# Optimization experiments

Hardware: AMD Instinct MI355X
Metric: run time of the kernel (lower is better)

## Reference

```python
import jax, jax.numpy as jnp
import numpy as np

B = 64            # decode batch (one new token per sequence)
H = 32            # query heads
HKV = 2           # kv heads (multi_query_group_num)
D = 128           # head_size (kv_channels)
HID = 4096        # hidden size
ROT = D // 2      # ChatGLM applies rotary to first half of head dims
BLOCK = 16        # paged-cache block size
NBLK = 16384      # total blocks
MAX_S = 4096
ROPE_BASE = 10000.0


def setup_inputs() -> dict:
    key = jax.random.key(0)
    ks = jax.random.split(key, 8)
    hidden_states = jax.random.normal(ks[0], (B, HID), jnp.float32)
    wqkv = jax.random.normal(ks[1], (H * D + 2 * HKV * D, HID), jnp.float32) * 0.02
    wdense = jax.random.normal(ks[2], (HID, H * D), jnp.float32) * 0.02
    k_cache = jax.random.normal(ks[3], (NBLK, BLOCK, HKV, D), jnp.float32)
    v_cache = jax.random.normal(ks[4], (NBLK, BLOCK, HKV, D), jnp.float32)
    # disjoint block tables: sequence b owns blocks [b*256, (b+1)*256)
    block_tables = jnp.arange(B * (MAX_S // BLOCK), dtype=jnp.int32).reshape(B, MAX_S // BLOCK)
    input_lengths = jax.random.randint(ks[5], (B,), 1024, MAX_S + 1, dtype=jnp.int32)
    # slot of the current token = position input_lengths-1 within its block table
    pos = input_lengths - 1
    slots = block_tables[jnp.arange(B), pos // BLOCK] * BLOCK + pos % BLOCK
    return {"hidden_states": hidden_states, "wqkv": wqkv, "wdense": wdense,
            "k_cache": k_cache, "v_cache": v_cache, "block_tables": block_tables,
            "slots": slots, "input_lengths": input_lengths, "max_s": MAX_S}


def _apply_rope(x, positions):
    # x: [B, h, D]; GPT-J interleaved rope on first ROT dims (ChatGLM style)
    inv_freq = 1.0 / (ROPE_BASE ** (jnp.arange(0, ROT, 2, dtype=jnp.float32) / ROT))  # [ROT/2]
    ang = positions.astype(jnp.float32)[:, None] * inv_freq[None, :]                  # [B, ROT/2]
    c = jnp.cos(ang)[:, None, :]  # [B,1,ROT/2]
    s = jnp.sin(ang)[:, None, :]
    xr = x[..., :ROT].reshape(*x.shape[:-1], ROT // 2, 2)
    x0, x1 = xr[..., 0], xr[..., 1]
    rot = jnp.stack([x0 * c - x1 * s, x1 * c + x0 * s], axis=-1).reshape(*x.shape[:-1], ROT)
    return jnp.concatenate([rot, x[..., ROT:]], axis=-1)


def reference(hidden_states, wqkv, wdense, k_cache, v_cache, block_tables, slots, input_lengths, max_s):
    G = H // HKV
    scale = D ** -0.5
    positions = input_lengths - 1

    qkv = hidden_states @ wqkv.T                                   # [B, 4608]
    q, k, v = jnp.split(qkv, [H * D, H * D + HKV * D], axis=1)
    q = q.reshape(B, H, D)
    k = k.reshape(B, HKV, D)
    v = v.reshape(B, HKV, D)

    q = _apply_rope(q, positions)
    k = _apply_rope(k, positions)

    # reshape_and_cache: scatter current token's K/V into the paged cache
    kc = k_cache.reshape(NBLK * BLOCK, HKV, D).at[slots].set(k)
    vc = v_cache.reshape(NBLK * BLOCK, HKV, D).at[slots].set(v)

    # paged attention: gather per-sequence KV via block tables
    s_idx = jnp.arange(max_s)
    flat = block_tables[:, s_idx // BLOCK] * BLOCK + s_idx % BLOCK  # [B, S]
    K = kc[flat]                                                    # [B, S, HKV, D]
    V = vc[flat]

    q4 = q.reshape(B, HKV, G, D).astype(jnp.float32)
    scores = jnp.einsum('bkgd,bskd->bkgs', q4, K.astype(jnp.float32)) * scale  # [B,HKV,G,S]
    mask = s_idx[None, :] < input_lengths[:, None]                  # [B, S]
    scores = jnp.where(mask[:, None, None, :], scores, -jnp.inf)
    probs = jax.nn.softmax(scores, axis=-1)
    out = jnp.einsum('bkgs,bskd->bkgd', probs, V.astype(jnp.float32))  # [B,HKV,G,D]
    out = out.reshape(B, H * D).astype(hidden_states.dtype)
    return out @ wdense.T
```

## Files before the change

kernel.cpp:

```cpp
#include <hip/hip_runtime.h>
#include <math.h>

#define KDIM 4096
#define SPLITS 8
#define WAYS 32
#define MAXPB 256
#define NQKV 4608
#define NDENSE 4096
#define KSPLIT 8
#define KRANGE 512

typedef __attribute__((ext_vector_type(8))) short bh8;
typedef __attribute__((ext_vector_type(4))) float f32x4;

__device__ __forceinline__ short f2bf(float x) {
    union { float f; unsigned u; } v; v.f = x;
    unsigned r = v.u + 0x7FFFu + ((v.u >> 16) & 1u);
    return (short)(r >> 16);
}
__device__ __forceinline__ float bf2f(short h) {
    union { unsigned u; float f; } v;
    v.u = ((unsigned)(unsigned short)h) << 16;
    return v.f;
}

__device__ __forceinline__ void rope_rotate(float& x0, float& x1, int j, int pos) {
    double inv = pow(10000.0, -(double)j / 32.0);
    double ang = (double)pos * inv;
    float c = (float)cos(ang), s = (float)sin(ang);
    float r0 = x0 * c - x1 * s;
    float r1 = x1 * c + x0 * s;
    x0 = r0; x1 = r1;
}

__global__ __launch_bounds__(256) void prep_hilo(
    const float* __restrict__ x, unsigned short* __restrict__ hi,
    unsigned short* __restrict__ lo)
{
    const int i = (blockIdx.x * 256 + threadIdx.x) * 4;
    float4 v = *(const float4*)&x[i];
    unsigned short h4[4], l4[4];
    float vf[4] = {v.x, v.y, v.z, v.w};
    #pragma unroll
    for (int j = 0; j < 4; ++j) {
        short hh = f2bf(vf[j]);
        h4[j] = (unsigned short)hh;
        l4[j] = (unsigned short)f2bf(vf[j] - bf2f(hh));
    }
    *(ushort4*)&hi[i] = make_ushort4(h4[0], h4[1], h4[2], h4[3]);
    *(ushort4*)&lo[i] = make_ushort4(l4[0], l4[1], l4[2], l4[3]);
}

__global__ __launch_bounds__(256) void gemm_mfma(
    const unsigned short* __restrict__ A_hi, const unsigned short* __restrict__ A_lo,
    const float* __restrict__ W, float* __restrict__ part, int N)
{
    const int tid = threadIdx.x;
    const int wv = tid >> 6;
    const int l = tid & 63;
    const int lr = l & 15;
    const int h = l >> 4;
    const int n0 = blockIdx.x * 64 + wv * 16;
    const int k0 = blockIdx.y * KRANGE;

    const float* wrow = &W[(size_t)(n0 + lr) * KDIM + h * 8];
    const unsigned short* pah[4];
    const unsigned short* pal[4];
    #pragma unroll
    for (int mt = 0; mt < 4; ++mt) {
        pah[mt] = &A_hi[(mt * 16 + lr) * KDIM + h * 8];
        pal[mt] = &A_lo[(mt * 16 + lr) * KDIM + h * 8];
    }

    f32x4 acc[4];
    #pragma unroll
    for (int mt = 0; mt < 4; ++mt) acc[mt] = (f32x4){0.f, 0.f, 0.f, 0.f};

    float4 wc0, wc1, wn0, wn1;
    bh8 ahc[4], alc[4], ahn[4], aln[4];

    wc0 = *(const float4*)&wrow[k0];
    wc1 = *(const float4*)&wrow[k0 + 4];
    #pragma unroll
    for (int mt = 0; mt < 4; ++mt) {
        ahc[mt] = *(const bh8*)&pah[mt][k0];
        alc[mt] = *(const bh8*)&pal[mt][k0];
    }

    for (int kt = 0; kt < KRANGE / 32; ++kt) {
        if (kt + 1 < KRANGE / 32) {
            const int kn = k0 + (kt + 1) * 32;
            wn0 = *(const float4*)&wrow[kn];
            wn1 = *(const float4*)&wrow[kn + 4];
            #pragma unroll
            for (int mt = 0; mt < 4; ++mt) {
                ahn[mt] = *(const bh8*)&pah[mt][kn];
                aln[mt] = *(const bh8*)&pal[mt][kn];
            }
        }
        bh8 whi, wlo;
        float wf[8] = {wc0.x, wc0.y, wc0.z, wc0.w, wc1.x, wc1.y, wc1.z, wc1.w};
        #pragma unroll
        for (int e = 0; e < 8; ++e) {
            short hh = f2bf(wf[e]);
            whi[e] = hh;
            wlo[e] = f2bf(wf[e] - bf2f(hh));
        }
        #pragma unroll
        for (int mt = 0; mt < 4; ++mt) {
            acc[mt] = __builtin_amdgcn_mfma_f32_16x16x32_bf16(ahc[mt], whi, acc[mt], 0, 0, 0);
            acc[mt] = __builtin_amdgcn_mfma_f32_16x16x32_bf16(alc[mt], whi, acc[mt], 0, 0, 0);
            acc[mt] = __builtin_amdgcn_mfma_f32_16x16x32_bf16(ahc[mt], wlo, acc[mt], 0, 0, 0);
        }
        wc0 = wn0; wc1 = wn1;
        #pragma unroll
        for (int mt = 0; mt < 4; ++mt) { ahc[mt] = ahn[mt]; alc[mt] = aln[mt]; }
    }

    const int ks = blockIdx.y;
    #pragma unroll
    for (int mt = 0; mt < 4; ++mt) {
        const int m = mt * 16 + h * 4;
        #pragma unroll
        for (int j = 0; j < 4; ++j)
            part[((size_t)ks * 64 + m + j) * N + n0 + lr] = acc[mt][j];
    }
}

__global__ __launch_bounds__(256) void reduce_qkv(
    const float* __restrict__ part, const int* __restrict__ lens,
    float* __restrict__ q_rope, float* __restrict__ knew, float* __restrict__ vnew)
{
    const int b = blockIdx.y;
    const int c0 = (blockIdx.x * 256 + threadIdx.x) * 2;
    float x0 = 0.f, x1 = 0.f;
    #pragma unroll
    for (int ks = 0; ks < KSPLIT; ++ks) {
        float2 v = *(const float2*)&part[((size_t)ks * 64 + b) * NQKV + c0];
        x0 += v.x; x1 += v.y;
    }
    const int pos = lens[b] - 1;
    if (c0 < 4096) {
        const int d = c0 & 127;
        if (d < 64) rope_rotate(x0, x1, d >> 1, pos);
        q_rope[(size_t)b * 4096 + c0] = x0;
        q_rope[(size_t)b * 4096 + c0 + 1] = x1;
    } else if (c0 < 4352) {
        const int kidx = c0 - 4096, kh = kidx >> 7, d = kidx & 127;
        if (d < 64) rope_rotate(x0, x1, d >> 1, pos);
        knew[(b * 2 + kh) * 128 + d] = x0;
        knew[(b * 2 + kh) * 128 + d + 1] = x1;
    } else {
        const int vidx = c0 - 4352, kh = vidx >> 7, d = vidx & 127;
        vnew[(b * 2 + kh) * 128 + d] = x0;
        vnew[(b * 2 + kh) * 128 + d + 1] = x1;
    }
}

__global__ __launch_bounds__(256) void attn_mfma(
    const float* __restrict__ qr, const float* __restrict__ knew,
    const float* __restrict__ vnew, const float* __restrict__ kcache,
    const float* __restrict__ vcache, const int* __restrict__ bt,
    const int* __restrict__ lens, float* __restrict__ pO, float* __restrict__ pML)
{
    const int split = blockIdx.x;
    const int kh = blockIdx.y;
    const int b = blockIdx.z;
    const int tid = threadIdx.x;
    const int wv = tid >> 6;
    const int l = tid & 63;
    const int g = l & 15;
    const int h = l >> 4;
    const int way = split * 4 + wv;

    __shared__ unsigned int sP[4][256];
    __shared__ float sO[3][16][132];
    __shared__ float sML[3][2][16];

    const int len = lens[b];
    const int nchunks = (len + 31) >> 5;
    const size_t nbase = ((size_t)(b * 2 + kh)) * 128;

    const float scale = 0.08838834764831845f;
    bh8 qf[4];
    {
        const float* qrow = &qr[((size_t)(b * 32 + kh * 16 + g)) * 128 + h * 8];
        #pragma unroll
        for (int dc = 0; dc < 4; ++dc) {
            float4 a = *(const float4*)&qrow[dc * 32];
            float4 c = *(const float4*)&qrow[dc * 32 + 4];
            qf[dc][0] = f2bf(a.x * scale); qf[dc][1] = f2bf(a.y * scale);
            qf[dc][2] = f2bf(a.z * scale); qf[dc][3] = f2bf(a.w * scale);
            qf[dc][4] = f2bf(c.x * scale); qf[dc][5] = f2bf(c.y * scale);
            qf[dc][6] = f2bf(c.z * scale); qf[dc][7] = f2bf(c.w * scale);
        }
    }

    float m = -INFINITY, lacc = 0.f;
    f32x4 oacc[8];
    #pragma unroll
    for (int dt = 0; dt < 8; ++dt) oacc[dt] = (f32x4){0.f, 0.f, 0.f, 0.f};

    for (int c = way; c < nchunks; c += WAYS) {
        const int s0 = c * 32;
        const int blk0 = bt[b * MAXPB + 2 * c];
        const int blk1 = bt[b * MAXPB + 2 * c + 1];

        const float* rowK0 = (s0 + g == len - 1) ? &knew[nbase]
            : &kcache[(((size_t)blk0 * 16 + g) * 2 + kh) * 128];
        const float* rowK1 = (s0 + 16 + g == len - 1) ? &knew[nbase]
            : &kcache[(((size_t)blk1 * 16 + g) * 2 + kh) * 128];
        float4 k0[8], k1[8];
        #pragma unroll
        for (int dc = 0; dc < 4; ++dc) {
            k0[2*dc]   = *(const float4*)&rowK0[dc * 32 + h * 8];
            k0[2*dc+1] = *(const float4*)&rowK0[dc * 32 + h * 8 + 4];
            k1[2*dc]   = *(const float4*)&rowK1[dc * 32 + h * 8];
            k1[2*dc+1] = *(const float4*)&rowK1[dc * 32 + h * 8 + 4];
        }

        float vv[8][8];
        #pragma unroll
        for (int e = 0; e < 8; ++e) {
            const int p = h * 8 + e;
            const int s = s0 + p;
            const float* rowV = (s == len - 1) ? &vnew[nbase]
                : &vcache[(((size_t)(p < 16 ? blk0 : blk1) * 16 + (p & 15)) * 2 + kh) * 128];
            #pragma unroll
            for (int dt = 0; dt < 8; ++dt)
                vv[e][dt] = rowV[dt * 16 + g];
        }

        f32x4 sa0 = (f32x4){0.f,0.f,0.f,0.f};
        f32x4 sa1 = (f32x4){0.f,0.f,0.f,0.f};
        #pragma unroll
        for (int dc = 0; dc < 4; ++dc) {
            bh8 a0, a1;
            a0[0]=f2bf(k0[2*dc].x);   a0[1]=f2bf(k0[2*dc].y);
            a0[2]=f2bf(k0[2*dc].z);   a0[3]=f2bf(k0[2*dc].w);
            a0[4]=f2bf(k0[2*dc+1].x); a0[5]=f2bf(k0[2*dc+1].y);
            a0[6]=f2bf(k0[2*dc+1].z); a0[7]=f2bf(k0[2*dc+1].w);
            a1[0]=f2bf(k1[2*dc].x);   a1[1]=f2bf(k1[2*dc].y);
            a1[2]=f2bf(k1[2*dc].z);   a1[3]=f2bf(k1[2*dc].w);
            a1[4]=f2bf(k1[2*dc+1].x); a1[5]=f2bf(k1[2*dc+1].y);
            a1[6]=f2bf(k1[2*dc+1].z); a1[7]=f2bf(k1[2*dc+1].w);
            sa0 = __builtin_amdgcn_mfma_f32_16x16x32_bf16(a0, qf[dc], sa0, 0, 0, 0);
            sa1 = __builtin_amdgcn_mfma_f32_16x16x32_bf16(a1, qf[dc], sa1, 0, 0, 0);
        }

        float sc[8];
        #pragma unroll
        for (int j = 0; j < 4; ++j) {
            sc[j]     = (s0 + 4*h + j      < len) ? sa0[j] : -INFINITY;
            sc[4 + j] = (s0 + 16 + 4*h + j < len) ? sa1[j] : -INFINITY;
        }
        float tmax = sc[0];
        #pragma unroll
        for (int j = 1; j < 8; ++j) tmax = fmaxf(tmax, sc[j]);
        tmax = fmaxf(tmax, __shfl_xor(tmax, 16));
        tmax = fmaxf(tmax, __shfl_xor(tmax, 32));
        const float m_new = fmaxf(m, tmax);
        const float corr = expf(m - m_new);
        float pe[8], ls = 0.f;
        #pragma unroll
        for (int j = 0; j < 8; ++j) { pe[j] = expf(sc[j] - m_new); ls += pe[j]; }
        ls += __shfl_xor(ls, 16);
        ls += __shfl_xor(ls, 32);
        lacc = lacc * corr + ls;
        m = m_new;
        #pragma unroll
        for (int dt = 0; dt < 8; ++dt) {
            oacc[dt][0] *= corr; oacc[dt][1] *= corr;
            oacc[dt][2] *= corr; oacc[dt][3] *= corr;
        }

        unsigned int* myP = sP[wv];
        #pragma unroll
        for (int ph = 0; ph < 2; ++ph)
            #pragma unroll
            for (int t2 = 0; t2 < 2; ++t2) {
                unsigned lo = (unsigned short)f2bf(pe[ph*4 + 2*t2]);
                unsigned hi = (unsigned short)f2bf(pe[ph*4 + 2*t2 + 1]);
                myP[g * 16 + ph * 8 + 2 * h + t2] = lo | (hi << 16);
            }
        asm volatile("s_waitcnt lgkmcnt(0)" ::: "memory");
        bh8 pf = *(const bh8*)&myP[g * 16 + 4 * h];

        #pragma unroll
        for (int dt = 0; dt < 8; ++dt) {
            bh8 av;
            #pragma unroll
            for (int e = 0; e < 8; ++e) av[e] = f2bf(vv[e][dt]);
            oacc[dt] = __builtin_amdgcn_mfma_f32_16x16x32_bf16(av, pf, oacc[dt], 0, 0, 0);
        }
    }

    if (wv > 0) {
        #pragma unroll
        for (int dt = 0; dt < 8; ++dt)
            #pragma unroll
            for (int j = 0; j < 4; ++j)
                sO[wv-1][g][dt*16 + 4*h + j] = oacc[dt][j];
        if (l < 16) {
            sML[wv-1][0][g] = m;
            sML[wv-1][1][g] = lacc;
        }
    }
    __syncthreads();
    if (wv == 0) {
        float M = m;
        #pragma unroll
        for (int i = 0; i < 3; ++i) M = fmaxf(M, sML[i][0][g]);
        const float w0 = expf(m - M);
        float L = lacc * w0;
        float wi[3];
        #pragma unroll
        for (int i = 0; i < 3; ++i) {
            wi[i] = expf(sML[i][0][g] - M);
            L += sML[i][1][g] * wi[i];
        }
        size_t base = ((((size_t)(b * 2 + kh)) * SPLITS + split) * 16 + g) * 128;
        #pragma unroll
        for (int dt = 0; dt < 8; ++dt)
            #pragma unroll
            for (int j = 0; j < 4; ++j) {
                float o = oacc[dt][j] * w0;
                #pragma unroll
                for (int i = 0; i < 3; ++i)
                    o += sO[i][g][dt*16 + 4*h + j] * wi[i];
                pO[base + dt*16 + 4*h + j] = o;
            }
        if (l < 16) {
            size_t mb = ((((size_t)(b * 2 + kh)) * SPLITS + split) * 16 + g) * 2;
            pML[mb] = M;
            pML[mb + 1] = L;
        }
    }
}

__global__ __launch_bounds__(256) void attn_combine(
    const float* __restrict__ pO, const float* __restrict__ pML,
    unsigned short* __restrict__ a_hi, unsigned short* __restrict__ a_lo)
{
    const int bk = blockIdx.x;
    const int tid = threadIdx.x;
    const int g = tid >> 4;
    const int dh = tid & 15;

    float ms[SPLITS], ls[SPLITS];
    float M = -INFINITY;
    #pragma unroll
    for (int s = 0; s < SPLITS; ++s) {
        size_t mb = (((size_t)bk * SPLITS + s) * 16 + g) * 2;
        ms[s] = pML[mb]; ls[s] = pML[mb + 1];
        M = fmaxf(M, ms[s]);
    }
    float L = 0.f;
    #pragma unroll
    for (int s = 0; s < SPLITS; ++s) L += ls[s] * expf(ms[s] - M);

    float acc[8] = {0, 0, 0, 0, 0, 0, 0, 0};
    #pragma unroll
    for (int s = 0; s < SPLITS; ++s) {
        float wgt = expf(ms[s] - M);
        const float* src = &pO[(((size_t)bk * SPLITS + s) * 16 + g) * 128 + dh * 8];
        #pragma unroll
        for (int r = 0; r < 8; ++r) acc[r] += wgt * src[r];
    }
    const float invL = 1.f / L;
    const int b = bk >> 1, kh = bk & 1;
    const size_t idx = (size_t)b * 4096 + (kh * 16 + g) * 128 + dh * 8;
    unsigned short hbuf[8], lbuf[8];
    #pragma unroll
    for (int r = 0; r < 8; ++r) {
        float o = acc[r] * invL;
        short hh = f2bf(o);
        hbuf[r] = (unsigned short)hh;
        lbuf[r] = (unsigned short)f2bf(o - bf2f(hh));
    }
    *(int4*)&a_hi[idx] = *(int4*)hbuf;
    *(int4*)&a_lo[idx] = *(int4*)lbuf;
}

__global__ __launch_bounds__(256) void reduce_dense(
    const float* __restrict__ part, float* __restrict__ out)
{
    const int b = blockIdx.y;
    const int col = (blockIdx.x * 256 + threadIdx.x) * 4;
    float4 s = make_float4(0.f, 0.f, 0.f, 0.f);
    #pragma unroll
    for (int ks = 0; ks < KSPLIT; ++ks) {
        float4 v = *(const float4*)&part[((size_t)ks * 64 + b) * NDENSE + col];
        s.x += v.x; s.y += v.y; s.z += v.z; s.w += v.w;
    }
    *(float4*)&out[(size_t)b * 4096 + col] = s;
}

extern "C" void kernel_launch(void* const* d_in, const int* in_sizes, int n_in,
                              void* d_out, int out_size, void* d_ws, size_t ws_size,
                              hipStream_t stream) {
    const float* hidden = (const float*)d_in[0];
    const float* wqkv   = (const float*)d_in[1];
    const float* wdense = (const float*)d_in[2];
    const float* kcache = (const float*)d_in[3];
    const float* vcache = (const float*)d_in[4];
    const int*   bt     = (const int*)d_in[5];
    const int*   lens   = (const int*)d_in[7];
    float* out = (float*)d_out;

    float* ws     = (float*)d_ws;
    float* q_rope = ws;
    float* k_new  = ws + 262144;
    float* v_new  = ws + 278528;
    unsigned short* hiloA = (unsigned short*)(ws + 294912);
    unsigned short* A_hi = hiloA;
    unsigned short* A_lo = hiloA + 262144;
    float* regX   = ws + 557056;
    float* pO     = regX;
    float* pML    = ws + 2916352;

    prep_hilo<<<dim3(256), dim3(256), 0, stream>>>(hidden, A_hi, A_lo);
    gemm_mfma<<<dim3(NQKV / 64, KSPLIT), dim3(256), 0, stream>>>(
        A_hi, A_lo, wqkv, regX, NQKV);
    reduce_qkv<<<dim3(9, 64), dim3(256), 0, stream>>>(
        regX, lens, q_rope, k_new, v_new);
    attn_mfma<<<dim3(SPLITS, 2, 64), dim3(256), 0, stream>>>(
        q_rope, k_new, v_new, kcache, vcache, bt, lens, pO, pML);
    attn_combine<<<dim3(128), dim3(256), 0, stream>>>(pO, pML, A_hi, A_lo);
    gemm_mfma<<<dim3(NDENSE / 64, KSPLIT), dim3(256), 0, stream>>>(
        A_hi, A_lo, wdense, regX, NDENSE);
    reduce_dense<<<dim3(4, 64), dim3(256), 0, stream>>>(regX, out);
}
```

Measured before the change: 211.5 us.

## Prefetch next K chunk in attention loop and double GEMM split-K

The attention loop is software-pipelined. K for the next chunk is loaded into registers while the current chunk's bf16 conversion and MFMA run, and V loads are issued earlier in the iteration. The projection GEMMs use twice as many K-splits with half the range each, giving more blocks in flight, and both kernels gain occupancy hints in launch_bounds. The costs are more partial-sum traffic and reduction work in the reduce kernels, a larger workspace (pML is moved), and higher register pressure that could cause spills.

```diff
diff --git a/kernel.cpp b/kernel.cpp
--- a/kernel.cpp
+++ b/kernel.cpp
@@ -7,8 +7,8 @@
 #define MAXPB 256
 #define NQKV 4608
 #define NDENSE 4096
-#define KSPLIT 8
-#define KRANGE 512
+#define KSPLIT 16
+#define KRANGE 256
 
 typedef __attribute__((ext_vector_type(8))) short bh8;
 typedef __attribute__((ext_vector_type(4))) float f32x4;
@@ -51,7 +51,7 @@
     *(ushort4*)&lo[i] = make_ushort4(l4[0], l4[1], l4[2], l4[3]);
 }
 
-__global__ __launch_bounds__(256) void gemm_mfma(
+__global__ __launch_bounds__(256, 3) void gemm_mfma(
     const unsigned short* __restrict__ A_hi, const unsigned short* __restrict__ A_lo,
     const float* __restrict__ W, float* __restrict__ part, int N)
 {
@@ -157,7 +157,7 @@
     }
 }
 
-__global__ __launch_bounds__(256) void attn_mfma(
+__global__ __launch_bounds__(256, 2) void attn_mfma(
     const float* __restrict__ qr, const float* __restrict__ knew,
     const float* __restrict__ vnew, const float* __restrict__ kcache,
     const float* __restrict__ vcache, const int* __restrict__ bt,
@@ -201,25 +201,29 @@
     #pragma unroll
     for (int dt = 0; dt < 8; ++dt) oacc[dt] = (f32x4){0.f, 0.f, 0.f, 0.f};
 
-    for (int c = way; c < nchunks; c += WAYS) {
+    float4 kst0[8], kst1[8];
+    float vv[8][8];
+
+    auto issueK = [&](int c) {
         const int s0 = c * 32;
         const int blk0 = bt[b * MAXPB + 2 * c];
         const int blk1 = bt[b * MAXPB + 2 * c + 1];
-
         const float* rowK0 = (s0 + g == len - 1) ? &knew[nbase]
             : &kcache[(((size_t)blk0 * 16 + g) * 2 + kh) * 128];
         const float* rowK1 = (s0 + 16 + g == len - 1) ? &knew[nbase]
             : &kcache[(((size_t)blk1 * 16 + g) * 2 + kh) * 128];
-        float4 k0[8], k1[8];
         #pragma unroll
         for (int dc = 0; dc < 4; ++dc) {
-            k0[2*dc]   = *(const float4*)&rowK0[dc * 32 + h * 8];
-            k0[2*dc+1] = *(const float4*)&rowK0[dc * 32 + h * 8 + 4];
-            k1[2*dc]   = *(const float4*)&rowK1[dc * 32 + h * 8];
-            k1[2*dc+1] = *(const float4*)&rowK1[dc * 32 + h * 8 + 4];
-        }
-
-        float vv[8][8];
+            kst0[2*dc]   = *(const float4*)&rowK0[dc * 32 + h * 8];
+            kst0[2*dc+1] = *(const float4*)&rowK0[dc * 32 + h * 8 + 4];
+            kst1[2*dc]   = *(const float4*)&rowK1[dc * 32 + h * 8];
+            kst1[2*dc+1] = *(const float4*)&rowK1[dc * 32 + h * 8 + 4];
+        }
+    };
+    auto issueV = [&](int c) {
+        const int s0 = c * 32;
+        const int blk0 = bt[b * MAXPB + 2 * c];
+        const int blk1 = bt[b * MAXPB + 2 * c + 1];
         #pragma unroll
         for (int e = 0; e < 8; ++e) {
             const int p = h * 8 + e;
@@ -230,22 +234,35 @@
             for (int dt = 0; dt < 8; ++dt)
                 vv[e][dt] = rowV[dt * 16 + g];
         }
+    };
+
+    issueK(way);
+
+    for (int c = way; c < nchunks; c += WAYS) {
+        const int s0 = c * 32;
+
+        bh8 a0[4], a1[4];
+        #pragma unroll
+        for (int dc = 0; dc < 4; ++dc) {
+            a0[dc][0]=f2bf(kst0[2*dc].x);   a0[dc][1]=f2bf(kst0[2*dc].y);
+            a0[dc][2]=f2bf(kst0[2*dc].z);   a0[dc][3]=f2bf(kst0[2*dc].w);
+            a0[dc][4]=f2bf(kst0[2*dc+1].x); a0[dc][5]=f2bf(kst0[2*dc+1].y);
+            a0[dc][6]=f2bf(kst0[2*dc+1].z); a0[dc][7]=f2bf(kst0[2*dc+1].w);
+            a1[dc][0]=f2bf(kst1[2*dc].x);   a1[dc][1]=f2bf(kst1[2*dc].y);
+            a1[dc][2]=f2bf(kst1[2*dc].z);   a1[dc][3]=f2bf(kst1[2*dc].w);
+            a1[dc][4]=f2bf(kst1[2*dc+1].x); a1[dc][5]=f2bf(kst1[2*dc+1].y);
+            a1[dc][6]=f2bf(kst1[2*dc+1].z); a1[dc][7]=f2bf(kst1[2*dc+1].w);
+        }
+
+        issueV(c);
+        if (c + WAYS < nchunks) issueK(c + WAYS);
 
         f32x4 sa0 = (f32x4){0.f,0.f,0.f,0.f};
         f32x4 sa1 = (f32x4){0.f,0.f,0.f,0.f};
         #pragma unroll
         for (int dc = 0; dc < 4; ++dc) {
-            bh8 a0, a1;
-            a0[0]=f2bf(k0[2*dc].x);   a0[1]=f2bf(k0[2*dc].y);
-            a0[2]=f2bf(k0[2*dc].z);   a0[3]=f2bf(k0[2*dc].w);
-            a0[4]=f2bf(k0[2*dc+1].x); a0[5]=f2bf(k0[2*dc+1].y);
-            a0[6]=f2bf(k0[2*dc+1].z); a0[7]=f2bf(k0[2*dc+1].w);
-            a1[0]=f2bf(k1[2*dc].x);   a1[1]=f2bf(k1[2*dc].y);
-            a1[2]=f2bf(k1[2*dc].z);   a1[3]=f2bf(k1[2*dc].w);
-            a1[4]=f2bf(k1[2*dc+1].x); a1[5]=f2bf(k1[2*dc+1].y);
-            a1[6]=f2bf(k1[2*dc+1].z); a1[7]=f2bf(k1[2*dc+1].w);
-            sa0 = __builtin_amdgcn_mfma_f32_16x16x32_bf16(a0, qf[dc], sa0, 0, 0, 0);
-            sa1 = __builtin_amdgcn_mfma_f32_16x16x32_bf16(a1, qf[dc], sa1, 0, 0, 0);
+            sa0 = __builtin_amdgcn_mfma_f32_16x16x32_bf16(a0[dc], qf[dc], sa0, 0, 0, 0);
+            sa1 = __builtin_amdgcn_mfma_f32_16x16x32_bf16(a1[dc], qf[dc], sa1, 0, 0, 0);
         }
 
         float sc[8];
@@ -412,12 +429,11 @@
     float* q_rope = ws;
     float* k_new  = ws + 262144;
     float* v_new  = ws + 278528;
-    unsigned short* hiloA = (unsigned short*)(ws + 294912);
-    unsigned short* A_hi = hiloA;
-    unsigned short* A_lo = hiloA + 262144;
+    unsigned short* A_hi = (unsigned short*)(ws + 294912);
+    unsigned short* A_lo = A_hi + 262144;
     float* regX   = ws + 557056;
     float* pO     = regX;
-    float* pML    = ws + 2916352;
+    float* pML    = ws + 5275648;
 
     prep_hilo<<<dim3(256), dim3(256), 0, stream>>>(hidden, A_hi, A_lo);
     gemm_mfma<<<dim3(NQKV / 64, KSPLIT), dim3(256), 0, stream>>>(
```

New measurement: 234.3 us. +10.8%, slower.

## Split attention into one chunk per wave with early-exit empty blocks

Applied to the files above, without the earlier changes.

Grows the attention split count from 8 to 32 so every wave handles exactly one 32-token chunk, which drops the online-softmax rescale loop. Blocks whose chunks lie entirely past the sequence length write neutral max/sum values and return at once. The combine kernel now reduces 32 partials and skips those with zero weight. The aim is to raise occupancy and balance work across variable sequence lengths, at the cost of more partial-result traffic and a heavier combine step.

```diff
diff --git a/kernel.cpp b/kernel.cpp
--- a/kernel.cpp
+++ b/kernel.cpp
@@ -2,8 +2,7 @@
 #include <math.h>
 
 #define KDIM 4096
-#define SPLITS 8
-#define WAYS 32
+#define ASPL 32
 #define MAXPB 256
 #define NQKV 4608
 #define NDENSE 4096
@@ -171,7 +170,7 @@
     const int l = tid & 63;
     const int g = l & 15;
     const int h = l >> 4;
-    const int way = split * 4 + wv;
+    const int c = split * 4 + wv;
 
     __shared__ unsigned int sP[4][256];
     __shared__ float sO[3][16][132];
@@ -179,29 +178,39 @@
 
     const int len = lens[b];
     const int nchunks = (len + 31) >> 5;
+    const size_t mlbase = ((((size_t)(b * 2 + kh)) * ASPL + split) * 16) * 2;
+
+    if (split * 4 >= nchunks) {
+        if (wv == 0 && l < 16) {
+            pML[mlbase + g * 2] = -INFINITY;
+            pML[mlbase + g * 2 + 1] = 0.f;
+        }
+        return;
+    }
+
     const size_t nbase = ((size_t)(b * 2 + kh)) * 128;
-
     const float scale = 0.08838834764831845f;
-    bh8 qf[4];
-    {
-        const float* qrow = &qr[((size_t)(b * 32 + kh * 16 + g)) * 128 + h * 8];
-        #pragma unroll
-        for (int dc = 0; dc < 4; ++dc) {
-            float4 a = *(const float4*)&qrow[dc * 32];
-            float4 c = *(const float4*)&qrow[dc * 32 + 4];
-            qf[dc][0] = f2bf(a.x * scale); qf[dc][1] = f2bf(a.y * scale);
-            qf[dc][2] = f2bf(a.z * scale); qf[dc][3] = f2bf(a.w * scale);
-            qf[dc][4] = f2bf(c.x * scale); qf[dc][5] = f2bf(c.y * scale);
-            qf[dc][6] = f2bf(c.z * scale); qf[dc][7] = f2bf(c.w * scale);
-        }
-    }
 
     float m = -INFINITY, lacc = 0.f;
     f32x4 oacc[8];
     #pragma unroll
     for (int dt = 0; dt < 8; ++dt) oacc[dt] = (f32x4){0.f, 0.f, 0.f, 0.f};
 
-    for (int c = way; c < nchunks; c += WAYS) {
+    if (c < nchunks) {
+        bh8 qf[4];
+        {
+            const float* qrow = &qr[((size_t)(b * 32 + kh * 16 + g)) * 128 + h * 8];
+            #pragma unroll
+            for (int dc = 0; dc < 4; ++dc) {
+                float4 a = *(const float4*)&qrow[dc * 32];
+                float4 cc = *(const float4*)&qrow[dc * 32 + 4];
+                qf[dc][0] = f2bf(a.x * scale);  qf[dc][1] = f2bf(a.y * scale);
+                qf[dc][2] = f2bf(a.z * scale);  qf[dc][3] = f2bf(a.w * scale);
+                qf[dc][4] = f2bf(cc.x * scale); qf[dc][5] = f2bf(cc.y * scale);
+                qf[dc][6] = f2bf(cc.z * scale); qf[dc][7] = f2bf(cc.w * scale);
+            }
+        }
+
         const int s0 = c * 32;
         const int blk0 = bt[b * MAXPB + 2 * c];
         const int blk1 = bt[b * MAXPB + 2 * c + 1];
@@ -259,20 +268,13 @@
         for (int j = 1; j < 8; ++j) tmax = fmaxf(tmax, sc[j]);
         tmax = fmaxf(tmax, __shfl_xor(tmax, 16));
         tmax = fmaxf(tmax, __shfl_xor(tmax, 32));
-        const float m_new = fmaxf(m, tmax);
-        const float corr = expf(m - m_new);
+        m = tmax;
         float pe[8], ls = 0.f;
         #pragma unroll
-        for (int j = 0; j < 8; ++j) { pe[j] = expf(sc[j] - m_new); ls += pe[j]; }
+        for (int j = 0; j < 8; ++j) { pe[j] = expf(sc[j] - m); ls += pe[j]; }
         ls += __shfl_xor(ls, 16);
         ls += __shfl_xor(ls, 32);
-        lacc = lacc * corr + ls;
-        m = m_new;
-        #pragma unroll
-        for (int dt = 0; dt < 8; ++dt) {
-            oacc[dt][0] *= corr; oacc[dt][1] *= corr;
-            oacc[dt][2] *= corr; oacc[dt][3] *= corr;
-        }
+        lacc = ls;
 
         unsigned int* myP = sP[wv];
         #pragma unroll
@@ -319,7 +321,7 @@
             wi[i] = expf(sML[i][0][g] - M);
             L += sML[i][1][g] * wi[i];
         }
-        size_t base = ((((size_t)(b * 2 + kh)) * SPLITS + split) * 16 + g) * 128;
+        size_t base = ((((size_t)(b * 2 + kh)) * ASPL + split) * 16 + g) * 128;
         #pragma unroll
         for (int dt = 0; dt < 8; ++dt)
             #pragma unroll
@@ -331,9 +333,8 @@
                 pO[base + dt*16 + 4*h + j] = o;
             }
         if (l < 16) {
-            size_t mb = ((((size_t)(b * 2 + kh)) * SPLITS + split) * 16 + g) * 2;
-            pML[mb] = M;
-            pML[mb + 1] = L;
+            pML[mlbase + g * 2] = M;
+            pML[mlbase + g * 2 + 1] = L;
         }
     }
 }
@@ -347,25 +348,27 @@
     const int g = tid >> 4;
     const int dh = tid & 15;
 
-    float ms[SPLITS], ls[SPLITS];
+    float ms[ASPL], ls[ASPL];
     float M = -INFINITY;
     #pragma unroll
-    for (int s = 0; s < SPLITS; ++s) {
-        size_t mb = (((size_t)bk * SPLITS + s) * 16 + g) * 2;
+    for (int s = 0; s < ASPL; ++s) {
+        size_t mb = (((size_t)bk * ASPL + s) * 16 + g) * 2;
         ms[s] = pML[mb]; ls[s] = pML[mb + 1];
         M = fmaxf(M, ms[s]);
     }
     float L = 0.f;
     #pragma unroll
-    for (int s = 0; s < SPLITS; ++s) L += ls[s] * expf(ms[s] - M);
+    for (int s = 0; s < ASPL; ++s) L += ls[s] * expf(ms[s] - M);
 
     float acc[8] = {0, 0, 0, 0, 0, 0, 0, 0};
     #pragma unroll
-    for (int s = 0; s < SPLITS; ++s) {
+    for (int s = 0; s < ASPL; ++s) {
         float wgt = expf(ms[s] - M);
-        const float* src = &pO[(((size_t)bk * SPLITS + s) * 16 + g) * 128 + dh * 8];
-        #pragma unroll
-        for (int r = 0; r < 8; ++r) acc[r] += wgt * src[r];
+        if (wgt > 0.f) {
+            const float* src = &pO[(((size_t)bk * ASPL + s) * 16 + g) * 128 + dh * 8];
+            #pragma unroll
+            for (int r = 0; r < 8; ++r) acc[r] += wgt * src[r];
+        }
     }
     const float invL = 1.f / L;
     const int b = bk >> 1, kh = bk & 1;
@@ -412,19 +415,18 @@
     float* q_rope = ws;
     float* k_new  = ws + 262144;
     float* v_new  = ws + 278528;
-    unsigned short* hiloA = (unsigned short*)(ws + 294912);
-    unsigned short* A_hi = hiloA;
-    unsigned short* A_lo = hiloA + 262144;
+    unsigned short* A_hi = (unsigned short*)(ws + 294912);
+    unsigned short* A_lo = A_hi + 262144;
     float* regX   = ws + 557056;
     float* pO     = regX;
-    float* pML    = ws + 2916352;
+    float* pML    = ws + 557056 + 8388608;
 
     prep_hilo<<<dim3(256), dim3(256), 0, stream>>>(hidden, A_hi, A_lo);
     gemm_mfma<<<dim3(NQKV / 64, KSPLIT), dim3(256), 0, stream>>>(
         A_hi, A_lo, wqkv, regX, NQKV);
     reduce_qkv<<<dim3(9, 64), dim3(256), 0, stream>>>(
         regX, lens, q_rope, k_new, v_new);
-    attn_mfma<<<dim3(SPLITS, 2, 64), dim3(256), 0, stream>>>(
+    attn_mfma<<<dim3(ASPL, 2, 64), dim3(256), 0, stream>>>(
         q_rope, k_new, v_new, kcache, vcache, bt, lens, pO, pML);
     attn_combine<<<dim3(128), dim3(256), 0, stream>>>(pO, pML, A_hi, A_lo);
     gemm_mfma<<<dim3(NDENSE / 64, KSPLIT), dim3(256), 0, stream>>>(
```

New measurement: 219.9 us. 4.0% more time.

## Fuse split-K reduction and RoPE into GEMMs via intra-block LDS reduction

Applied to the files above, without the earlier changes.

The GEMM now gives each block 16 output columns, and its four waves each cover a quarter of K. Partial sums are reduced through shared memory inside the block, which removes the separate reduce_qkv and reduce_dense kernels and their global partial-sum traffic. RoPE and the q/k/v scatter are applied in the QKV GEMM epilogue, using a lane shuffle to fetch the paired element. The grid changes from 72x8 to 288 blocks for QKV and 256 for dense, so there is less parallelism per block, and the epilogue runs serially in wave 0.

```diff
diff --git a/kernel.cpp b/kernel.cpp
--- a/kernel.cpp
+++ b/kernel.cpp
@@ -7,8 +7,6 @@
 #define MAXPB 256
 #define NQKV 4608
 #define NDENSE 4096
-#define KSPLIT 8
-#define KRANGE 512
 
 typedef __attribute__((ext_vector_type(8))) short bh8;
 typedef __attribute__((ext_vector_type(4))) float f32x4;
@@ -22,15 +20,6 @@
     union { unsigned u; float f; } v;
     v.u = ((unsigned)(unsigned short)h) << 16;
     return v.f;
-}
-
-__device__ __forceinline__ void rope_rotate(float& x0, float& x1, int j, int pos) {
-    double inv = pow(10000.0, -(double)j / 32.0);
-    double ang = (double)pos * inv;
-    float c = (float)cos(ang), s = (float)sin(ang);
-    float r0 = x0 * c - x1 * s;
-    float r1 = x1 * c + x0 * s;
-    x0 = r0; x1 = r1;
 }
 
 __global__ __launch_bounds__(256) void prep_hilo(
@@ -51,17 +40,20 @@
     *(ushort4*)&lo[i] = make_ushort4(l4[0], l4[1], l4[2], l4[3]);
 }
 
-__global__ __launch_bounds__(256) void gemm_mfma(
+template<int MODE>
+__global__ __launch_bounds__(256) void gemm_fused(
     const unsigned short* __restrict__ A_hi, const unsigned short* __restrict__ A_lo,
-    const float* __restrict__ W, float* __restrict__ part, int N)
+    const float* __restrict__ W, const int* __restrict__ lens,
+    float* __restrict__ oq, float* __restrict__ ok, float* __restrict__ ov)
 {
+    __shared__ float sM[3][64][16];
     const int tid = threadIdx.x;
     const int wv = tid >> 6;
     const int l = tid & 63;
     const int lr = l & 15;
     const int h = l >> 4;
-    const int n0 = blockIdx.x * 64 + wv * 16;
-    const int k0 = blockIdx.y * KRANGE;
+    const int n0 = blockIdx.x * 16;
+    const int kbase = wv * 1024;
 
     const float* wrow = &W[(size_t)(n0 + lr) * KDIM + h * 8];
     const unsigned short* pah[4];
@@ -76,30 +68,33 @@
     #pragma unroll
     for (int mt = 0; mt < 4; ++mt) acc[mt] = (f32x4){0.f, 0.f, 0.f, 0.f};
 
-    float4 wc0, wc1, wn0, wn1;
+    float4 wa0, wb0, wa1, wb1;
     bh8 ahc[4], alc[4], ahn[4], aln[4];
-
-    wc0 = *(const float4*)&wrow[k0];
-    wc1 = *(const float4*)&wrow[k0 + 4];
+    wa0 = *(const float4*)&wrow[kbase];
+    wb0 = *(const float4*)&wrow[kbase + 4];
+    wa1 = *(const float4*)&wrow[kbase + 32];
+    wb1 = *(const float4*)&wrow[kbase + 36];
     #pragma unroll
     for (int mt = 0; mt < 4; ++mt) {
-        ahc[mt] = *(const bh8*)&pah[mt][k0];
-        alc[mt] = *(const bh8*)&pal[mt][k0];
-    }
-
-    for (int kt = 0; kt < KRANGE / 32; ++kt) {
-        if (kt + 1 < KRANGE / 32) {
-            const int kn = k0 + (kt + 1) * 32;
-            wn0 = *(const float4*)&wrow[kn];
-            wn1 = *(const float4*)&wrow[kn + 4];
+        ahc[mt] = *(const bh8*)&pah[mt][kbase];
+        alc[mt] = *(const bh8*)&pal[mt][kbase];
+    }
+
+    auto body = [&](float4& pwa, float4& pwb, int kcur) {
+        float4 cw0 = pwa, cw1 = pwb;
+        if (kcur + 64 < 1024) {
+            pwa = *(const float4*)&wrow[kbase + kcur + 64];
+            pwb = *(const float4*)&wrow[kbase + kcur + 68];
+        }
+        if (kcur + 32 < 1024) {
             #pragma unroll
             for (int mt = 0; mt < 4; ++mt) {
-                ahn[mt] = *(const bh8*)&pah[mt][kn];
-                aln[mt] = *(const bh8*)&pal[mt][kn];
+                ahn[mt] = *(const bh8*)&pah[mt][kbase + kcur + 32];
+                aln[mt] = *(const bh8*)&pal[mt][kbase + kcur + 32];
             }
         }
         bh8 whi, wlo;
-        float wf[8] = {wc0.x, wc0.y, wc0.z, wc0.w, wc1.x, wc1.y, wc1.z, wc1.w};
+        float wf[8] = {cw0.x, cw0.y, cw0.z, cw0.w, cw1.x, cw1.y, cw1.z, cw1.w};
         #pragma unroll
         for (int e = 0; e < 8; ++e) {
             short hh = f2bf(wf[e]);
@@ -112,48 +107,61 @@
             acc[mt] = __builtin_amdgcn_mfma_f32_16x16x32_bf16(alc[mt], whi, acc[mt], 0, 0, 0);
             acc[mt] = __builtin_amdgcn_mfma_f32_16x16x32_bf16(ahc[mt], wlo, acc[mt], 0, 0, 0);
         }
-        wc0 = wn0; wc1 = wn1;
-        #pragma unroll
-        for (int mt = 0; mt < 4; ++mt) { ahc[mt] = ahn[mt]; alc[mt] = aln[mt]; }
-    }
-
-    const int ks = blockIdx.y;
-    #pragma unroll
-    for (int mt = 0; mt < 4; ++mt) {
-        const int m = mt * 16 + h * 4;
-        #pragma unroll
-        for (int j = 0; j < 4; ++j)
-            part[((size_t)ks * 64 + m + j) * N + n0 + lr] = acc[mt][j];
-    }
-}
-
-__global__ __launch_bounds__(256) void reduce_qkv(
-    const float* __restrict__ part, const int* __restrict__ lens,
-    float* __restrict__ q_rope, float* __restrict__ knew, float* __restrict__ vnew)
-{
-    const int b = blockIdx.y;
-    const int c0 = (blockIdx.x * 256 + threadIdx.x) * 2;
-    float x0 = 0.f, x1 = 0.f;
-    #pragma unroll
-    for (int ks = 0; ks < KSPLIT; ++ks) {
-        float2 v = *(const float2*)&part[((size_t)ks * 64 + b) * NQKV + c0];
-        x0 += v.x; x1 += v.y;
-    }
-    const int pos = lens[b] - 1;
-    if (c0 < 4096) {
-        const int d = c0 & 127;
-        if (d < 64) rope_rotate(x0, x1, d >> 1, pos);
-        q_rope[(size_t)b * 4096 + c0] = x0;
-        q_rope[(size_t)b * 4096 + c0 + 1] = x1;
-    } else if (c0 < 4352) {
-        const int kidx = c0 - 4096, kh = kidx >> 7, d = kidx & 127;
-        if (d < 64) rope_rotate(x0, x1, d >> 1, pos);
-        knew[(b * 2 + kh) * 128 + d] = x0;
-        knew[(b * 2 + kh) * 128 + d + 1] = x1;
-    } else {
-        const int vidx = c0 - 4352, kh = vidx >> 7, d = vidx & 127;
-        vnew[(b * 2 + kh) * 128 + d] = x0;
-        vnew[(b * 2 + kh) * 128 + d + 1] = x1;
+        if (kcur + 32 < 1024) {
+            #pragma unroll
+            for (int mt = 0; mt < 4; ++mt) { ahc[mt] = ahn[mt]; alc[mt] = aln[mt]; }
+        }
+    };
+
+    for (int kt2 = 0; kt2 < 16; ++kt2) {
+        body(wa0, wb0, kt2 * 64);
+        body(wa1, wb1, kt2 * 64 + 32);
+    }
+
+    if (wv > 0) {
+        #pragma unroll
+        for (int mt = 0; mt < 4; ++mt)
+            #pragma unroll
+            for (int j = 0; j < 4; ++j)
+                sM[wv - 1][mt * 16 + h * 4 + j][lr] = acc[mt][j];
+    }
+    __syncthreads();
+    if (wv == 0) {
+        const int n = n0 + lr;
+        #pragma unroll
+        for (int mt = 0; mt < 4; ++mt) {
+            #pragma unroll
+            for (int j = 0; j < 4; ++j) {
+                const int m = mt * 16 + h * 4 + j;
+                float x = acc[mt][j] + sM[0][m][lr] + sM[1][m][lr] + sM[2][m][lr];
+                if (MODE == 1) {
+                    oq[(size_t)m * 4096 + n] = x;
+                } else {
+                    if (n < 4352) {
+                        const int d = n & 127;
+                        float xo = __shfl_xor(x, 1);
+                        float xr = x;
+                        if (d < 64) {
+                            const int pos = lens[m] - 1;
+                            double inv = pow(10000.0, -(double)(d >> 1) / 32.0);
+                            double ang = (double)pos * inv;
+                            float cc = (float)cos(ang), ss = (float)sin(ang);
+                            xr = ((d & 1) == 0) ? (x * cc - xo * ss)
+                                                : (x * cc + xo * ss);
+                        }
+                        if (n < 4096) {
+                            oq[(size_t)m * 4096 + n] = xr;
+                        } else {
+                            const int kk = n - 4096;
+                            ok[(m * 2 + (kk >> 7)) * 128 + (kk & 127)] = xr;
+                        }
+                    } else {
+                        const int vv2 = n - 4352;
+                        ov[(m * 2 + (vv2 >> 7)) * 128 + (vv2 & 127)] = x;
+                    }
+                }
+            }
+        }
     }
 }
 
@@ -382,20 +390,6 @@
     *(int4*)&a_lo[idx] = *(int4*)lbuf;
 }
 
-__global__ __launch_bounds__(256) void reduce_dense(
-    const float* __restrict__ part, float* __restrict__ out)
-{
-    const int b = blockIdx.y;
-    const int col = (blockIdx.x * 256 + threadIdx.x) * 4;
-    float4 s = make_float4(0.f, 0.f, 0.f, 0.f);
-    #pragma unroll
-    for (int ks = 0; ks < KSPLIT; ++ks) {
-        float4 v = *(const float4*)&part[((size_t)ks * 64 + b) * NDENSE + col];
-        s.x += v.x; s.y += v.y; s.z += v.z; s.w += v.w;
-    }
-    *(float4*)&out[(size_t)b * 4096 + col] = s;
-}
-
 extern "C" void kernel_launch(void* const* d_in, const int* in_sizes, int n_in,
                               void* d_out, int out_size, void* d_ws, size_t ws_size,
                               hipStream_t stream) {
@@ -412,22 +406,17 @@
     float* q_rope = ws;
     float* k_new  = ws + 262144;
     float* v_new  = ws + 278528;
-    unsigned short* hiloA = (unsigned short*)(ws + 294912);
-    unsigned short* A_hi = hiloA;
-    unsigned short* A_lo = hiloA + 262144;
-    float* regX   = ws + 557056;
-    float* pO     = regX;
-    float* pML    = ws + 2916352;
+    unsigned short* A_hi = (unsigned short*)(ws + 294912);
+    unsigned short* A_lo = A_hi + 262144;
+    float* pO     = ws + 557056;
+    float* pML    = ws + 2654208;
 
     prep_hilo<<<dim3(256), dim3(256), 0, stream>>>(hidden, A_hi, A_lo);
-    gemm_mfma<<<dim3(NQKV / 64, KSPLIT), dim3(256), 0, stream>>>(
-        A_hi, A_lo, wqkv, regX, NQKV);
-    reduce_qkv<<<dim3(9, 64), dim3(256), 0, stream>>>(
-        regX, lens, q_rope, k_new, v_new);
+    gemm_fused<0><<<dim3(NQKV / 16), dim3(256), 0, stream>>>(
+        A_hi, A_lo, wqkv, lens, q_rope, k_new, v_new);
     attn_mfma<<<dim3(SPLITS, 2, 64), dim3(256), 0, stream>>>(
         q_rope, k_new, v_new, kcache, vcache, bt, lens, pO, pML);
     attn_combine<<<dim3(128), dim3(256), 0, stream>>>(pO, pML, A_hi, A_lo);
-    gemm_mfma<<<dim3(NDENSE / 64, KSPLIT), dim3(256), 0, stream>>>(
-        A_hi, A_lo, wdense, regX, NDENSE);
-    reduce_dense<<<dim3(4, 64), dim3(256), 0, stream>>>(regX, out);
-}
+    gemm_fused<1><<<dim3(NDENSE / 16), dim3(256), 0, stream>>>(
+        A_hi, A_lo, wdense, nullptr, out, nullptr, nullptr);
+}
```

New measurement: 234.7 us. 10.9% more time.
